# Performance work log

Measured on AMD Instinct MI355X. Metric: run time of the kernel, lower is better.

## Reference

```python
import jax, jax.numpy as jnp
import numpy as np

E, H, B, S = 512, 8, 8, 1024  # embed_dim, n_head, batch, n_agent (sequence)
DH = E // H
DECAY_SCALING = 1.0


def _rmsnorm(x, scale, eps=1e-6):
    return x * jax.lax.rsqrt(jnp.mean(x * x, axis=-1, keepdims=True) + eps) * scale


def _groupnorm(y, scale, bias, n_head, eps=1e-5):
    # GroupNorm with num_groups = n_head over the feature axis (flax semantics).
    b, s, e = y.shape
    yg = y.reshape(b, s, n_head, e // n_head)
    mu = jnp.mean(yg, axis=-1, keepdims=True)
    var = jnp.var(yg, axis=-1, keepdims=True)
    yn = (yg - mu) * jax.lax.rsqrt(var + eps)
    return yn.reshape(b, s, e) * scale + bias


def _decay_kappas(n_head, scaling):
    # RetNet multi-scale decays: 1 - exp(linspace(log(1/32), log(1/512), H))
    k = 1.0 - jnp.exp(jnp.linspace(jnp.log(1.0 / 32.0), jnp.log(1.0 / 512.0), n_head))
    return (k * scaling).astype(jnp.float32)


def _msr(key_x, query_x, value_x, wq, wk, wv, wg, wo, gs, gb, kappas):
    # Parallel multi-scale retention (masked / causal, full_self_retention=False).
    b, s, e = query_x.shape
    h = wq.shape[0]
    q = jnp.einsum('bse,hed->bhsd', query_x, wq)
    k = jnp.einsum('bse,hed->bhsd', key_x, wk)
    v = jnp.einsum('bse,hed->bhsd', value_x, wv)
    n = jnp.arange(s)
    diff = n[:, None] - n[None, :]
    causal = diff >= 0
    expnt = jnp.where(causal, diff, 0).astype(q.dtype)
    # D[h,n,m] = kappa_h^(n-m) for n>=m else 0
    D = jnp.where(causal[None], kappas[:, None, None] ** expnt[None], 0.0)
    scores = jnp.einsum('bhnd,bhmd->bhnm', q, k) * D[None]  # [B,H,S,S]
    ret = jnp.einsum('bhnm,bhmd->bhnd', scores, v)
    ret = ret.transpose(0, 2, 1, 3).reshape(b, s, e)
    ret = _groupnorm(ret, gs, gb, h)
    return (jax.nn.swish(query_x @ wg) * ret) @ wo


def _swiglu(x, w_gate, w_lin, w_out):
    return (jax.nn.swish(x @ w_gate) * (x @ w_lin)) @ w_out


def setup_inputs() -> dict:
    key = jax.random.key(0)
    ks = jax.random.split(key, 20)
    sc = 0.02
    d = {
        'x': jax.random.normal(ks[0], (B, S, E), jnp.float32),
        'obs_rep': jax.random.normal(ks[1], (B, S, E), jnp.float32),
        # retention 1 params
        'wq1': jax.random.normal(ks[2], (H, E, DH), jnp.float32) * sc,
        'wk1': jax.random.normal(ks[3], (H, E, DH), jnp.float32) * sc,
        'wv1': jax.random.normal(ks[4], (H, E, DH), jnp.float32) * sc,
        'wg1': jax.random.normal(ks[5], (E, E), jnp.float32) * sc,
        'wo1': jax.random.normal(ks[6], (E, E), jnp.float32) * sc,
        'gs1': jnp.ones((E,), jnp.float32),
        'gb1': jnp.zeros((E,), jnp.float32),
        # retention 2 params
        'wq2': jax.random.normal(ks[7], (H, E, DH), jnp.float32) * sc,
        'wk2': jax.random.normal(ks[8], (H, E, DH), jnp.float32) * sc,
        'wv2': jax.random.normal(ks[9], (H, E, DH), jnp.float32) * sc,
        'wg2': jax.random.normal(ks[10], (E, E), jnp.float32) * sc,
        'wo2': jax.random.normal(ks[11], (E, E), jnp.float32) * sc,
        'gs2': jnp.ones((E,), jnp.float32),
        'gb2': jnp.zeros((E,), jnp.float32),
        # RMSNorm scales
        'ln1_s': jnp.ones((E,), jnp.float32),
        'ln2_s': jnp.ones((E,), jnp.float32),
        'ln3_s': jnp.ones((E,), jnp.float32),
        # SwiGLU(hidden=E, input=E)
        'ffn_w_lin': jax.random.normal(ks[12], (E, E), jnp.float32) * sc,
        'ffn_w_gate': jax.random.normal(ks[13], (E, E), jnp.float32) * sc,
        'ffn_w_out': jax.random.normal(ks[14], (E, E), jnp.float32) * sc,
    }
    return d


def reference(x, obs_rep, wq1, wk1, wv1, wg1, wo1, gs1, gb1,
              wq2, wk2, wv2, wg2, wo2, gs2, gb2,
              ln1_s, ln2_s, ln3_s, ffn_w_lin, ffn_w_gate, ffn_w_out):
    kappas = _decay_kappas(H, DECAY_SCALING)
    # x = ln1(x + retn1(key=x, query=x, value=x))
    x1 = _rmsnorm(x + _msr(x, x, x, wq1, wk1, wv1, wg1, wo1, gs1, gb1, kappas), ln1_s)
    # x = ln2(obs_rep + retn2(key=x1, query=obs_rep, value=x1))
    x2 = _rmsnorm(obs_rep + _msr(x1, obs_rep, x1, wq2, wk2, wv2, wg2, wo2, gs2, gb2, kappas), ln2_s)
    # out = ln3(x2 + ffn(x2))
    return _rmsnorm(x2 + _swiglu(x2, ffn_w_gate, ffn_w_lin, ffn_w_out), ln3_s)
```

## Files before the change

### kernel.cpp

```cpp
#include <hip/hip_runtime.h>
#include <hip/hip_bf16.h>
#include <stdint.h>

typedef unsigned short u16;
typedef unsigned int   u32;
typedef __bf16 bf16x8 __attribute__((ext_vector_type(8)));
typedef u16    u16x8  __attribute__((ext_vector_type(8)));
typedef float  f32x4  __attribute__((ext_vector_type(4)));

#define E_   512
#define H_   8
#define DH_  64
#define B_   8
#define S_   1024
#define M_   (B_ * S_)
#define NTOT (M_ * E_)

__device__ __forceinline__ u16 f2bf(float f) {
    u32 x = __float_as_uint(f);
    x += 0x7fffu + ((x >> 16) & 1u);
    return (u16)(x >> 16);
}
__device__ __forceinline__ float bf2f(u16 b) { return __uint_as_float((u32)b << 16); }
__device__ __forceinline__ bf16x8 as_bf(u16x8 v) {
// ... 16 lines not shown
__global__ __launch_bounds__(256) void prep_weights(
    const float* __restrict__ wq1, const float* __restrict__ wk1, const float* __restrict__ wv1,
    const float* __restrict__ wg1, const float* __restrict__ wq2, const float* __restrict__ wk2,
    const float* __restrict__ wv2, const float* __restrict__ wg2, const float* __restrict__ wgat,
    const float* __restrict__ wlin, const float* __restrict__ wo1, const float* __restrict__ wo2,
    const float* __restrict__ wout,
    u16* __restrict__ WC1, u16* __restrict__ WC2, u16* __restrict__ WF,
    u16* __restrict__ WO1t, u16* __restrict__ WO2t, u16* __restrict__ WOUt) {
    __shared__ float tle[64][65];
    const int rt = blockIdx.y, c0 = blockIdx.x * 64, tid = threadIdx.x;
    u16* dst; const float* src; int lr0; bool qkv = false; int nb0 = 0, h = 0;
    if (rt < 64) {
        bool s1 = rt < 32;
        dst = s1 ? WC1 : WC2;
        int r = (rt & 31) * 64; lr0 = r;
        if (r < 1536) {
            qkv = true; h = (r >> 6) & 7;
            src = (r < 512) ? (s1 ? wq1 : wq2) : (r < 1024) ? (s1 ? wk1 : wk2) : (s1 ? wv1 : wv2);
        } else { src = s1 ? wg1 : wg2; nb0 = r - 1536; }
    } else if (rt < 80) {
        dst = WF; int r = (rt - 64) * 64; lr0 = r;
        src = (r < 512) ? wgat : wlin; nb0 = r & 511;
    } else if (rt < 88) { dst = WO1t; lr0 = (rt - 80) * 64; src = wo1; nb0 = lr0; }
    else if (rt < 96)   { dst = WO2t; lr0 = (rt - 88) * 64; src = wo2; nb0 = lr0; }
    else                { dst = WOUt; lr0 = (rt - 96) * 64; src = wout; nb0 = lr0; }

    #pragma unroll
    for (int i = 0; i < 16; ++i) {
        int idx = i * 256 + tid, a = idx >> 6, b = idx & 63;
        tle[a][b] = qkv ? src[(size_t)(h * 512 + c0 + a) * 64 + b]
                        : src[(size_t)(c0 + a) * 512 + nb0 + b];
    }
    __syncthreads();
    #pragma unroll
    for (int i = 0; i < 16; ++i) {
        int idx = i * 256 + tid;
        dst[(size_t)(lr0 + (idx >> 6)) * 512 + c0 + (idx & 63)] = f2bf(tle[idx & 63][idx >> 6]);
    }
}

__global__ __launch_bounds__(256) void cvt_both(const float* __restrict__ x,
                                                const float* __restrict__ obs,
                                                u16* __restrict__ XB, u16* __restrict__ OB) {
    int i = blockIdx.x * 256 + threadIdx.x;
    float4 v = ((const float4*)x)[i];
    ushort4 o;
    o.x = f2bf(v.x); o.y = f2bf(v.y); o.z = f2bf(v.z); o.w = f2bf(v.w);
    ((ushort4*)XB)[i] = o;
    v = ((const float4*)obs)[i];
    o.x = f2bf(v.x); o.y = f2bf(v.y); o.z = f2bf(v.z); o.w = f2bf(v.w);
    ((ushort4*)OB)[i] = o;
}

__global__ __launch_bounds__(256) void gemm_qkvg(const u16* __restrict__ A1,
                                                 const u16* __restrict__ A2,
                                                 const u16* __restrict__ W,
                                                 u16* __restrict__ QB, u16* __restrict__ KB,
                                                 u16* __restrict__ KT, u16* __restrict__ VT,
                                                 u16* __restrict__ GB) {
    __shared__ u16 sh[16384];
    u16* Als = sh;
    u16* Bls = sh + 8192;
    const int tid = threadIdx.x;
    const int l = tid & 63, w = tid >> 6;
    const int wm = w & 1, wn = w >> 1;
    int bx, by; xcd_map(blockIdx.x, 1024, 16, bx, by);
    const int bm = by * 128, bn = bx * 128;
    const int which = bx >> 2;
    const u16* A = (which == 1 || which == 2) ? A2 : A1;

    size_t srcA[4], srcB[4]; int ldst[4];
    #pragma unroll
    for (int c = 0; c < 4; ++c) {
        int row = c * 32 + w * 8 + (l >> 3);
        int chs = (l & 7) ^ (row & 7);
        srcA[c] = (size_t)(bm + row) * E_ + chs * 8;
        srcB[c] = (size_t)(bn + row) * E_ + chs * 8;
        ldst[c] = c * 2048 + w * 512;
    }
    int aoff[2][4], boff[2][4];
    #pragma unroll
    for (int kk = 0; kk < 2; ++kk)
        #pragma unroll
        for (int f = 0; f < 4; ++f) {
            int ra = wm * 64 + f * 16 + (l & 15);
            int rb = wn * 64 + f * 16 + (l & 15);
            int ch = kk * 4 + (l >> 4);
            aoff[kk][f] = ra * 128 + ((ch ^ (ra & 7)) << 4);
            boff[kk][f] = rb * 128 + ((ch ^ (rb & 7)) << 4);
        }

    f32x4 acc[4][4] = {};
    for (int t = 0; t < 8; ++t) {
        const int k1 = t * 64;
        #pragma unroll
        for (int c = 0; c < 4; ++c) {
            gll16(A + srcA[c] + k1, &Als[ldst[c]]);
            gll16(W + srcB[c] + k1, &Bls[ldst[c]]);
        }
        __syncthreads();
        #pragma unroll
        for (int kk = 0; kk < 2; ++kk) {
            bf16x8 af[4], bfr[4];
            #pragma unroll
            for (int f = 0; f < 4; ++f) {
                af[f]  = as_bf(*(const u16x8*)((const char*)Als + aoff[kk][f]));
                bfr[f] = as_bf(*(const u16x8*)((const char*)Bls + boff[kk][f]));
            }
            #pragma unroll
            for (int m = 0; m < 4; ++m)
                #pragma unroll
                for (int n = 0; n < 4; ++n)
                    acc[m][n] = __builtin_amdgcn_mfma_f32_16x16x32_bf16(af[m], bfr[n], acc[m][n], 0, 0, 0);
        }
        __syncthreads();
    }

    if (which != 2) {
        u16* dst = (which == 0) ? QB : (which == 1) ? KB : GB;
        #pragma unroll
        for (int m = 0; m < 4; ++m) {
            int row = bm + wm * 64 + m * 16 + ((l >> 4) << 2);
            #pragma unroll
            for (int n = 0; n < 4; ++n) {
                int coll = (bn & 511) + wn * 64 + n * 16 + (l & 15);
                f32x4 v = acc[m][n];
                #pragma unroll
                for (int r = 0; r < 4; ++r) dst[(size_t)(row + r) * E_ + coll] = f2bf(v[r]);
            }
        }
    }
    if (which == 1 || which == 2) {
        u16* dstT = (which == 2) ? VT : KT;
        #pragma unroll
        for (int m = 0; m < 4; ++m) {
            int row0 = wm * 64 + m * 16 + ((l >> 4) << 2);
            #pragma unroll
            for (int n = 0; n < 4; ++n) {
                int c = wn * 64 + n * 16 + (l & 15);
                f32x4 v = acc[m][n];
                uint2 pk; pk.x = cvtpk(v[0], v[1]); pk.y = cvtpk(v[2], v[3]);
                int off = c * 256 + (((row0 >> 3) ^ (c & 7)) << 4) + ((row0 & 7) << 1);
                *(uint2*)((char*)sh + off) = pk;
            }
        }
        __syncthreads();
        int c = tid >> 1, half = tid & 1;
        int collg = (bn & 511) + c;
        int bh = ((bm >> 10) << 3) + (collg >> 6);
        size_t gb = ((size_t)bh * 64 + (collg & 63)) * 1024 + (bm & 1023) + half * 64;
        #pragma unroll
        for (int j = 0; j < 8; ++j) {
            int chunk = half * 8 + j;
            uint4 vv = *(const uint4*)((const char*)sh + c * 256 + ((chunk ^ (c & 7)) << 4));
            *(uint4*)(dstT + gb + j * 8) = vv;
        }
    }
}

__global__ __launch_bounds__(256) void state_u(const u16* __restrict__ KT,
                                               const u16* __restrict__ VT,
                                               u16* __restrict__ U) {
    const int id = blockIdx.x;
    const int bh = id >> 3, c = id & 7;
    const int h = bh & 7;
    const int l = threadIdx.x & 63, w = threadIdx.x >> 6;
    const float kappa = 1.0f - __expf(-3.46573590f + (float)h * -0.39608410f);
    const float log2k = log2f(kappa);
    const float ik = 1.0f / kappa;

    bf16x8 af[4];
    {
        size_t vbase = ((size_t)bh * 64 + (w * 16 + (l & 15))) * 1024 + c * 128 + ((l >> 4) << 3);
        #pragma unroll
        for (int kk = 0; kk < 4; ++kk)
            af[kk] = as_bf(*(const u16x8*)(VT + vbase + kk * 32));
    }

    f32x4 acc[4] = {};
    #pragma unroll
    for (int fd = 0; fd < 4; ++fd) {
        size_t kbase = ((size_t)bh * 64 + (fd * 16 + (l & 15))) * 1024 + c * 128 + ((l >> 4) << 3);
        #pragma unroll
        for (int kk = 0; kk < 4; ++kk) {
            u16x8 kv = *(const u16x8*)(KT + kbase + kk * 32);
            int mb = kk * 32 + ((l >> 4) << 3);
            float wj = exp2f((float)(127 - mb) * log2k);
            u16x8 kw;
            #pragma unroll
            for (int j = 0; j < 8; ++j) { kw[j] = f2bf(bf2f(kv[j]) * wj); wj *= ik; }
            acc[fd] = __builtin_amdgcn_mfma_f32_16x16x32_bf16(af[kk], as_bf(kw), acc[fd], 0, 0, 0);
        }
    }

    #pragma unroll
    for (int fd = 0; fd < 4; ++fd) {
        int dv = w * 16 + ((l >> 4) << 2);
        int dk = fd * 16 + (l & 15);
        size_t ub = ((size_t)id * 64 + dv) * 64 + dk;
        #pragma unroll
        for (int r = 0; r < 4; ++r) U[ub + (size_t)r * 64] = f2bf(acc[fd][r]);
    }
}

__global__ __launch_bounds__(256) void retention_chunk(
        const u16* __restrict__ Q, const u16* __restrict__ K,
        const u16* __restrict__ VT, const u16* __restrict__ U,
        const u16* __restrict__ G,
        const float* __restrict__ gs, const float* __restrict__ gb,
        u16* __restrict__ T) {
    __shared__ u16 Ks[128 * 64], Vts[64 * 128], Ps[128 * 64], Ss[64 * 64];
    const int tid = threadIdx.x;
    const int l = tid & 63, w = tid >> 6;
    const int id = blockIdx.x;
    const int bh = id >> 3, c = id & 7;
    const int h = bh & 7;
    const int n0 = c * 128;
    const size_t base = (size_t)(bh >> 3) * (S_ * E_) + h * DH_;

    const float kappa = 1.0f - __expf(-3.46573590f + (float)h * -0.39608410f);
    const float log2k = log2f(kappa);
    const float ik = 1.0f / kappa;
    const float ikp2 = ik * ik, ikp3 = ikp2 * ik;

    float gsv[4], gbv[4];
    #pragma unroll
    for (int fd = 0; fd < 4; ++fd) {
        gsv[fd] = gs[h * 64 + fd * 16 + (l & 15)];
        gbv[fd] = gb[h * 64 + fd * 16 + (l & 15)];
    }

    #pragma unroll
    for (int cc = 0; cc < 4; ++cc) {
        int row = cc * 32 + w * 8 + (l >> 3);
        int chs = (l & 7) ^ (row & 7);
        gll16(K + base + (size_t)(n0 + row) * E_ + chs * 8, &Ks[cc * 2048 + w * 512]);
        int d = cc * 16 + w * 4 + (l >> 4);
        int vch = (l & 15) ^ (d & 15);
        gll16(VT + ((size_t)bh * 64 + d) * 1024 + n0 + vch * 8, &Vts[cc * 2048 + w * 512]);
    }

    bf16x8 qf[2][2];
    #pragma unroll
    for (int kk = 0; kk < 2; ++kk)
        #pragma unroll
        for (int fn = 0; fn < 2; ++fn) {
            int n = n0 + fn * 64 + w * 16 + (l & 15);
            qf[kk][fn] = as_bf(*(const u16x8*)(Q + base + (size_t)n * E_ + kk * 32 + ((l >> 4) << 3)));
        }

    if (c > 0) {
        float accs[16];
        #pragma unroll
        for (int j = 0; j < 16; ++j) accs[j] = 0.f;
        const float kC = exp2f(128.0f * log2k);
        float wc = 1.0f;
        size_t ub = (size_t)bh * (8 * 4096) + tid * 16;
        for (int cp = c - 1; cp >= 0; --cp) {
            const u16* up = U + ub + (size_t)cp * 4096;
            u16x8 a = *(const u16x8*)up;
            u16x8 b = *(const u16x8*)(up + 8);
            #pragma unroll
            for (int j = 0; j < 8; ++j) {
                accs[j]     += bf2f(a[j]) * wc;
                accs[8 + j] += bf2f(b[j]) * wc;
            }
            wc *= kC;
        }
        int dv = tid >> 2, ch0 = (tid & 3) << 1;
        #pragma unroll
        for (int hh = 0; hh < 2; ++hh) {
            uint4 pk;
            pk.x = cvtpk(accs[hh * 8 + 0], accs[hh * 8 + 1]);
            pk.y = cvtpk(accs[hh * 8 + 2], accs[hh * 8 + 3]);
            pk.z = cvtpk(accs[hh * 8 + 4], accs[hh * 8 + 5]);
            pk.w = cvtpk(accs[hh * 8 + 6], accs[hh * 8 + 7]);
            *(uint4*)((char*)Ss + dv * 128 + (((ch0 + hh) ^ (dv & 7)) << 4)) = pk;
        }
    }
    __syncthreads();

    f32x4 acc[2][4] = {};

    if (c > 0) {
        __builtin_amdgcn_s_setprio(1);
        #pragma unroll
        for (int kk = 0; kk < 2; ++kk) {
            bf16x8 sf[4];
            #pragma unroll
            for (int fd = 0; fd < 4; ++fd) {
                int dv = fd * 16 + (l & 15);
                int ch = kk * 4 + (l >> 4);
                sf[fd] = as_bf(*(const u16x8*)((const char*)Ss + dv * 128 + ((ch ^ (dv & 7)) << 4)));
            }
            #pragma unroll
            for (int fn = 0; fn < 2; ++fn)
                #pragma unroll
                for (int fd = 0; fd < 4; ++fd)
                    acc[fn][fd] = __builtin_amdgcn_mfma_f32_16x16x32_bf16(qf[kk][fn], sf[fd], acc[fn][fd], 0, 0, 0);
        }
        __builtin_amdgcn_s_setprio(0);
        #pragma unroll
        for (int fn = 0; fn < 2; ++fn) {
            int nl0 = fn * 64 + w * 16 + ((l >> 4) << 2);
            float fr0 = exp2f((float)(nl0 + 1) * log2k);
            float fr1 = fr0 * kappa, fr2 = fr1 * kappa, fr3 = fr2 * kappa;
            #pragma unroll
            for (int fd = 0; fd < 4; ++fd) {
                acc[fn][fd][0] *= fr0; acc[fn][fd][1] *= fr1;
                acc[fn][fd][2] *= fr2; acc[fn][fd][3] *= fr3;
            }
        }
    }

    #pragma unroll
    for (int mh = 0; mh < 2; ++mh) {
        const int m0l = mh * 64;
        bf16x8 kf[2][4];
        #pragma unroll
        for (int kk = 0; kk < 2; ++kk)
            #pragma unroll
            for (int f = 0; f < 4; ++f) {
                int row = m0l + f * 16 + (l & 15);
                int ch = kk * 4 + (l >> 4);
                kf[kk][f] = as_bf(*(const u16x8*)((const char*)Ks + row * 128 + ((ch ^ (row & 7)) << 4)));
            }
        #pragma unroll
        for (int fn = 0; fn < 2; ++fn) {
            if (mh == 1 && fn == 0) continue;
            f32x4 s[4] = {};
            __builtin_amdgcn_s_setprio(1);
            #pragma unroll
            for (int kk = 0; kk < 2; ++kk)
// ... 25 lines not shown
                pk.x = cvtpk(p0, p1);
                pk.y = cvtpk(p2, p3);
                *(uint2*)((char*)Ps + byteoff) = pk;
            }
        }
        #pragma unroll
        for (int km = 0; km < 2; ++km) {
            bf16x8 pf[2];
            #pragma unroll
            for (int fn = 0; fn < 2; ++fn) {
                if (mh == 1 && fn == 0) continue;
                int row = fn * 64 + w * 16 + (l & 15);
                int ch = km * 4 + (l >> 4);
                pf[fn] = as_bf(*(const u16x8*)((const char*)Ps + row * 128 + ((ch ^ (row & 7)) << 4)));
            }
            __builtin_amdgcn_s_setprio(1);
            #pragma unroll
            for (int fd = 0; fd < 4; ++fd) {
                int d = fd * 16 + (l & 15);
                int mch = mh * 8 + km * 4 + (l >> 4);
                bf16x8 vfr = as_bf(*(const u16x8*)((const char*)Vts + d * 256 + ((mch ^ (d & 15)) << 4)));
                #pragma unroll
                for (int fn = 0; fn < 2; ++fn) {
                    if (mh == 1 && fn == 0) continue;
                    acc[fn][fd] = __builtin_amdgcn_mfma_f32_16x16x32_bf16(pf[fn], vfr, acc[fn][fd], 0, 0, 0);
                }
            }
            __builtin_amdgcn_s_setprio(0);
        }
    }

    #pragma unroll
    for (int fn = 0; fn < 2; ++fn) {
        #pragma unroll
        for (int r = 0; r < 4; ++r) {
            float s1 = 0.f, s2 = 0.f;
            #pragma unroll
            for (int fd = 0; fd < 4; ++fd) { float v = acc[fn][fd][r]; s1 += v; s2 += v * v; }
            #pragma unroll
            for (int off = 1; off < 16; off <<= 1) {
                s1 += __shfl_xor(s1, off, 64);
                s2 += __shfl_xor(s2, off, 64);
            }
            float mean = s1 * (1.f / 64.f);
            float var  = s2 * (1.f / 64.f) - mean * mean;
            float rinv = rsqrtf(var + 1e-5f);
            int rowg = n0 + fn * 64 + w * 16 + ((l >> 4) << 2) + r;
            size_t rb = base + (size_t)rowg * E_;
            #pragma unroll
            for (int fd = 0; fd < 4; ++fd) {
                int d = fd * 16 + (l & 15);
                float ny = (acc[fn][fd][r] - mean) * rinv;
                float rn = ny * gsv[fd] + gbv[fd];
                float g = bf2f(G[rb + d]);
                T[rb + d] = f2bf(g * rn / (1.f + __expf(-g)));
            }
        }
    }
}

__global__ __launch_bounds__(256) void gemm_wo(const u16* __restrict__ A,
                                               const u16* __restrict__ W,
                                               u16* __restrict__ Cb) {
    __shared__ u16 Als[64 * 64];
    __shared__ u16 Bls[128 * 64];
    const int tid = threadIdx.x;
    const int l = tid & 63, w = tid >> 6;
    const int wm = w & 1, wn = w >> 1;
    int bx, by; xcd_map(blockIdx.x, 512, 4, bx, by);
    const int bm = by * 64, bn = bx * 128;

    size_t srcA[2], srcB[4]; int ldstA[2], ldstB[4];
    #pragma unroll
    for (int c = 0; c < 4; ++c) {
        int row = c * 32 + w * 8 + (l >> 3);
        int chs = (l & 7) ^ (row & 7);
        if (c < 2) { srcA[c] = (size_t)(bm + row) * E_ + chs * 8; ldstA[c] = c * 2048 + w * 512; }
        srcB[c] = (size_t)(bn + row) * E_ + chs * 8;
        ldstB[c] = c * 2048 + w * 512;
    }
    int aoff[2][2], boff[2][4];
    #pragma unroll
    for (int kk = 0; kk < 2; ++kk) {
        #pragma unroll
        for (int f = 0; f < 2; ++f) {
            int ra = wm * 32 + f * 16 + (l & 15);
            aoff[kk][f] = ra * 128 + (((kk * 4 + (l >> 4)) ^ (ra & 7)) << 4);
        }
        #pragma unroll
        for (int f = 0; f < 4; ++f) {
            int rb = wn * 64 + f * 16 + (l & 15);
            boff[kk][f] = rb * 128 + (((kk * 4 + (l >> 4)) ^ (rb & 7)) << 4);
        }
    }

    f32x4 acc[2][4] = {};
    for (int t = 0; t < 8; ++t) {
        const int k1 = t * 64;
        #pragma unroll
        for (int c = 0; c < 2; ++c) gll16(A + srcA[c] + k1, &Als[ldstA[c]]);
        #pragma unroll
        for (int c = 0; c < 4; ++c) gll16(W + srcB[c] + k1, &Bls[ldstB[c]]);
        __syncthreads();
        #pragma unroll
        for (int kk = 0; kk < 2; ++kk) {
            bf16x8 af[2], bfr[4];
            #pragma unroll
            for (int f = 0; f < 2; ++f) af[f] = as_bf(*(const u16x8*)((const char*)Als + aoff[kk][f]));
            #pragma unroll
            for (int f = 0; f < 4; ++f) bfr[f] = as_bf(*(const u16x8*)((const char*)Bls + boff[kk][f]));
            #pragma unroll
            for (int m = 0; m < 2; ++m)
                #pragma unroll
                for (int n = 0; n < 4; ++n)
                    acc[m][n] = __builtin_amdgcn_mfma_f32_16x16x32_bf16(af[m], bfr[n], acc[m][n], 0, 0, 0);
        }
        __syncthreads();
    }

    #pragma unroll
    for (int m = 0; m < 2; ++m) {
        int row = bm + wm * 32 + m * 16 + ((l >> 4) << 2);
        #pragma unroll
        for (int n = 0; n < 4; ++n) {
            int col = bn + wn * 64 + n * 16 + (l & 15);
            f32x4 v = acc[m][n];
            #pragma unroll
            for (int r = 0; r < 4; ++r) Cb[(size_t)(row + r) * E_ + col] = f2bf(v[r]);
        }
    }
}

__global__ __launch_bounds__(256) void gemm_ffn(const u16* __restrict__ A,
                                                const u16* __restrict__ W,
                                                u16* __restrict__ T) {
    __shared__ u16 Als[64 * 64];
    __shared__ u16 Bgs[64 * 64];
    __shared__ u16 Bls[64 * 64];
    const int tid = threadIdx.x;
    const int l = tid & 63, w = tid >> 6;
    const int wm = w & 1, wn = w >> 1;
    int bx, by; xcd_map(blockIdx.x, 1024, 8, bx, by);
    const int bm = by * 64, bn = bx * 64;

    size_t srcA[2], srcG[2], srcL[2]; int ldst[2];
    #pragma unroll
    for (int c = 0; c < 2; ++c) {
        int row = c * 32 + w * 8 + (l >> 3);
        int chs = (l & 7) ^ (row & 7);
        srcA[c] = (size_t)(bm + row) * E_ + chs * 8;
        srcG[c] = (size_t)(bn + row) * E_ + chs * 8;
        srcL[c] = (size_t)(512 + bn + row) * E_ + chs * 8;
        ldst[c] = c * 2048 + w * 512;
    }
    int aoff[2][2], goff[2][2];
    #pragma unroll
    for (int kk = 0; kk < 2; ++kk)
        #pragma unroll
        for (int f = 0; f < 2; ++f) {
            int ra = wm * 32 + f * 16 + (l & 15);
            int rb = wn * 32 + f * 16 + (l & 15);
            aoff[kk][f] = ra * 128 + (((kk * 4 + (l >> 4)) ^ (ra & 7)) << 4);
            goff[kk][f] = rb * 128 + (((kk * 4 + (l >> 4)) ^ (rb & 7)) << 4);
        }

    f32x4 accg[2][2] = {}, accl[2][2] = {};
    for (int t = 0; t < 8; ++t) {
        const int k1 = t * 64;
        #pragma unroll
        for (int c = 0; c < 2; ++c) {
            gll16(A + srcA[c] + k1, &Als[ldst[c]]);
            gll16(W + srcG[c] + k1, &Bgs[ldst[c]]);
            gll16(W + srcL[c] + k1, &Bls[ldst[c]]);
        }
        __syncthreads();
        #pragma unroll
        for (int kk = 0; kk < 2; ++kk) {
            bf16x8 af[2], bg[2], bl[2];
            #pragma unroll
            for (int f = 0; f < 2; ++f) {
                af[f] = as_bf(*(const u16x8*)((const char*)Als + aoff[kk][f]));
                bg[f] = as_bf(*(const u16x8*)((const char*)Bgs + goff[kk][f]));
                bl[f] = as_bf(*(const u16x8*)((const char*)Bls + goff[kk][f]));
            }
            #pragma unroll
            for (int m = 0; m < 2; ++m)
                #pragma unroll
                for (int n = 0; n < 2; ++n) {
                    accg[m][n] = __builtin_amdgcn_mfma_f32_16x16x32_bf16(af[m], bg[n], accg[m][n], 0, 0, 0);
                    accl[m][n] = __builtin_amdgcn_mfma_f32_16x16x32_bf16(af[m], bl[n], accl[m][n], 0, 0, 0);
                }
        }
        __syncthreads();
    }

    #pragma unroll
    for (int m = 0; m < 2; ++m) {
        int row = bm + wm * 32 + m * 16 + ((l >> 4) << 2);
        #pragma unroll
        for (int n = 0; n < 2; ++n) {
            int col = bn + wn * 32 + n * 16 + (l & 15);
            #pragma unroll
            for (int r = 0; r < 4; ++r) {
                float g = accg[m][n][r], lv = accl[m][n][r];
                T[(size_t)(row + r) * E_ + col] = f2bf(g * lv / (1.f + __expf(-g)));
            }
        }
    }
}

__global__ __launch_bounds__(512) void rmsnorm_res(const float* __restrict__ Xf,
                                                   const u16* __restrict__ Xb,
                                                   const u16* __restrict__ Yb,
                                                   const float* __restrict__ sc,
                                                   float* __restrict__ outf,
                                                   u16* __restrict__ outb) {
    __shared__ float part[8];
    size_t row = blockIdx.x;
    int t = threadIdx.x;
    float xv = Xf ? Xf[row * E_ + t] : bf2f(Xb[row * E_ + t]);
    float v = xv + bf2f(Yb[row * E_ + t]);
    float sq = v * v;
    #pragma unroll
    for (int off = 1; off < 64; off <<= 1) sq += __shfl_xor(sq, off, 64);
    if ((t & 63) == 0) part[t >> 6] = sq;
    __syncthreads();
    float tot = 0.0f;
    #pragma unroll
    for (int i = 0; i < 8; ++i) tot += part[i];
    float r = rsqrtf(tot * (1.0f / 512.0f) + 1e-6f);
    float o = v * r * sc[t];
    if (outf) outf[row * E_ + t] = o;
    if (outb) outb[row * E_ + t] = f2bf(o);
}

extern "C" void kernel_launch(void* const* d_in, const int* in_sizes, int n_in,
                              void* d_out, int out_size, void* d_ws, size_t ws_size,
                              hipStream_t stream) {
    const float* x    = (const float*)d_in[0];
    const float* obs  = (const float*)d_in[1];
    const float* wq1  = (const float*)d_in[2];
    const float* wk1  = (const float*)d_in[3];
    const float* wv1  = (const float*)d_in[4];
    const float* wg1  = (const float*)d_in[5];
    const float* wo1  = (const float*)d_in[6];
    const float* gs1  = (const float*)d_in[7];
    const float* gb1  = (const float*)d_in[8];
    const float* wq2  = (const float*)d_in[9];
    const float* wk2  = (const float*)d_in[10];
    const float* wv2  = (const float*)d_in[11];
    const float* wg2  = (const float*)d_in[12];
    const float* wo2  = (const float*)d_in[13];
    const float* gs2  = (const float*)d_in[14];
    const float* gb2  = (const float*)d_in[15];
    const float* ln1s = (const float*)d_in[16];
    const float* ln2s = (const float*)d_in[17];
    const float* ln3s = (const float*)d_in[18];
    const float* wlin = (const float*)d_in[19];
    const float* wgat = (const float*)d_in[20];
    const float* wout = (const float*)d_in[21];

    u16* wsb = (u16*)d_ws;
    u16* WC1  = wsb;
    u16* WC2  = WC1 + 2048 * 512;
    u16* WF   = WC2 + 2048 * 512;
    u16* WO1t = WF + 1024 * 512;
    u16* WO2t = WO1t + 512 * 512;
    u16* WOUt = WO2t + 512 * 512;
    u16* XB   = WOUt + 512 * 512;
    u16* OB   = XB + NTOT;
    u16* QB   = OB + NTOT;
    u16* KB   = QB + NTOT;
    u16* KT   = KB + NTOT;
    u16* VT   = KT + NTOT;
    u16* GB   = VT + NTOT;
    u16* TB   = GB + NTOT;
    u16* UB   = TB + NTOT;
    u16* YB   = QB;

    dim3 tG(256);

    prep_weights<<<dim3(8, 104), tG, 0, stream>>>(wq1, wk1, wv1, wg1, wq2, wk2, wv2, wg2,
                                                  wgat, wlin, wo1, wo2, wout,
                                                  WC1, WC2, WF, WO1t, WO2t, WOUt);
    cvt_both<<<NTOT / 1024, tG, 0, stream>>>(x, obs, XB, OB);

    gemm_qkvg<<<1024, tG, 0, stream>>>(XB, XB, WC1, QB, KB, KT, VT, GB);
    state_u<<<512, tG, 0, stream>>>(KT, VT, UB);
    retention_chunk<<<512, tG, 0, stream>>>(QB, KB, VT, UB, GB, gs1, gb1, TB);
    gemm_wo<<<512, tG, 0, stream>>>(TB, WO1t, YB);
    rmsnorm_res<<<M_, 512, 0, stream>>>(x, nullptr, YB, ln1s, nullptr, XB);

    gemm_qkvg<<<1024, tG, 0, stream>>>(OB, XB, WC2, QB, KB, KT, VT, GB);
    state_u<<<512, tG, 0, stream>>>(KT, VT, UB);
    retention_chunk<<<512, tG, 0, stream>>>(QB, KB, VT, UB, GB, gs2, gb2, TB);
    gemm_wo<<<512, tG, 0, stream>>>(TB, WO2t, YB);
    rmsnorm_res<<<M_, 512, 0, stream>>>(obs, nullptr, YB, ln2s, nullptr, OB);

    gemm_ffn<<<1024, tG, 0, stream>>>(OB, WF, TB);
    gemm_wo<<<512, tG, 0, stream>>>(TB, WOUt, YB);
    rmsnorm_res<<<M_, 512, 0, stream>>>(nullptr, OB, YB, ln3s, (float*)d_out, nullptr);
}
```

Baseline: 204.4 us.

## Fuse output projection GEMM with residual add and RMSNorm epilogue

Replaces the separate output-projection GEMM and row-wise RMSNorm kernels with one kernel. Each block computes full 512-wide rows for 32 rows, adds the residual and reduces the sum of squares across warps in shared memory, then writes the normalized output directly. This removes the intermediate bf16 projection buffer round trip and three kernel launches. In exchange it uses a large 64KB weight tile in LDS, launches only 256 blocks with lower occupancy, and adds MFMA priority hints.

```diff
diff --git a/kernel.cpp b/kernel.cpp
--- a/kernel.cpp
+++ b/kernel.cpp
@@ -457,74 +457,112 @@
     }
 }
 
-__global__ __launch_bounds__(256) void gemm_wo(const u16* __restrict__ A,
-                                               const u16* __restrict__ W,
-                                               u16* __restrict__ Cb) {
-    __shared__ u16 Als[64 * 64];
-    __shared__ u16 Bls[128 * 64];
+__global__ __launch_bounds__(256) void gemm_wo_rms(const u16* __restrict__ A,
+                                                   const u16* __restrict__ W,
+                                                   const float* __restrict__ Xf,
+                                                   const u16* __restrict__ Xb,
+                                                   const float* __restrict__ sc,
+                                                   float* __restrict__ outf,
+                                                   u16* __restrict__ outb) {
+    __shared__ u16 Bls[512 * 64];
+    __shared__ u16 Als[32 * 64];
+    __shared__ float red[4][32];
     const int tid = threadIdx.x;
     const int l = tid & 63, w = tid >> 6;
-    const int wm = w & 1, wn = w >> 1;
-    int bx, by; xcd_map(blockIdx.x, 512, 4, bx, by);
-    const int bm = by * 64, bn = bx * 128;
-
-    size_t srcA[2], srcB[4]; int ldstA[2], ldstB[4];
-    #pragma unroll
-    for (int c = 0; c < 4; ++c) {
+    const int bm = blockIdx.x * 32;
+
+    int arow = w * 8 + (l >> 3);
+    size_t srcA = (size_t)(bm + arow) * E_ + (((l & 7) ^ (arow & 7)) * 8);
+    int ldstA = w * 512;
+    size_t srcB[16]; int ldstB[16];
+    #pragma unroll
+    for (int c = 0; c < 16; ++c) {
         int row = c * 32 + w * 8 + (l >> 3);
-        int chs = (l & 7) ^ (row & 7);
-        if (c < 2) { srcA[c] = (size_t)(bm + row) * E_ + chs * 8; ldstA[c] = c * 2048 + w * 512; }
-        srcB[c] = (size_t)(bn + row) * E_ + chs * 8;
+        srcB[c] = (size_t)row * E_ + (((l & 7) ^ (row & 7)) * 8);
         ldstB[c] = c * 2048 + w * 512;
     }
-    int aoff[2][2], boff[2][4];
+    int aoff[2][2], boff[2][8];
     #pragma unroll
     for (int kk = 0; kk < 2; ++kk) {
         #pragma unroll
-        for (int f = 0; f < 2; ++f) {
-            int ra = wm * 32 + f * 16 + (l & 15);
-            aoff[kk][f] = ra * 128 + (((kk * 4 + (l >> 4)) ^ (ra & 7)) << 4);
-        }
-        #pragma unroll
-        for (int f = 0; f < 4; ++f) {
-            int rb = wn * 64 + f * 16 + (l & 15);
-            boff[kk][f] = rb * 128 + (((kk * 4 + (l >> 4)) ^ (rb & 7)) << 4);
-        }
-    }
-
-    f32x4 acc[2][4] = {};
+        for (int mi = 0; mi < 2; ++mi) {
+            int ra = mi * 16 + (l & 15);
+            aoff[kk][mi] = ra * 128 + (((kk * 4 + (l >> 4)) ^ (ra & 7)) << 4);
+        }
+        #pragma unroll
+        for (int n = 0; n < 8; ++n) {
+            int rb = w * 128 + n * 16 + (l & 15);
+            boff[kk][n] = rb * 128 + (((kk * 4 + (l >> 4)) ^ (rb & 7)) << 4);
+        }
+    }
+
+    f32x4 acc[2][8] = {};
     for (int t = 0; t < 8; ++t) {
         const int k1 = t * 64;
-        #pragma unroll
-        for (int c = 0; c < 2; ++c) gll16(A + srcA[c] + k1, &Als[ldstA[c]]);
-        #pragma unroll
-        for (int c = 0; c < 4; ++c) gll16(W + srcB[c] + k1, &Bls[ldstB[c]]);
+        gll16(A + srcA + k1, &Als[ldstA]);
+        #pragma unroll
+        for (int c = 0; c < 16; ++c) gll16(W + srcB[c] + k1, &Bls[ldstB[c]]);
         __syncthreads();
         #pragma unroll
         for (int kk = 0; kk < 2; ++kk) {
-            bf16x8 af[2], bfr[4];
-            #pragma unroll
-            for (int f = 0; f < 2; ++f) af[f] = as_bf(*(const u16x8*)((const char*)Als + aoff[kk][f]));
-            #pragma unroll
-            for (int f = 0; f < 4; ++f) bfr[f] = as_bf(*(const u16x8*)((const char*)Bls + boff[kk][f]));
-            #pragma unroll
-            for (int m = 0; m < 2; ++m)
+            bf16x8 af[2], bfr[8];
+            #pragma unroll
+            for (int mi = 0; mi < 2; ++mi)
+                af[mi] = as_bf(*(const u16x8*)((const char*)Als + aoff[kk][mi]));
+            #pragma unroll
+            for (int n = 0; n < 8; ++n)
+                bfr[n] = as_bf(*(const u16x8*)((const char*)Bls + boff[kk][n]));
+            __builtin_amdgcn_s_setprio(1);
+            #pragma unroll
+            for (int mi = 0; mi < 2; ++mi)
                 #pragma unroll
-                for (int n = 0; n < 4; ++n)
-                    acc[m][n] = __builtin_amdgcn_mfma_f32_16x16x32_bf16(af[m], bfr[n], acc[m][n], 0, 0, 0);
+                for (int n = 0; n < 8; ++n)
+                    acc[mi][n] = __builtin_amdgcn_mfma_f32_16x16x32_bf16(af[mi], bfr[n], acc[mi][n], 0, 0, 0);
+            __builtin_amdgcn_s_setprio(0);
         }
         __syncthreads();
     }
 
-    #pragma unroll
-    for (int m = 0; m < 2; ++m) {
-        int row = bm + wm * 32 + m * 16 + ((l >> 4) << 2);
-        #pragma unroll
-        for (int n = 0; n < 4; ++n) {
-            int col = bn + wn * 64 + n * 16 + (l & 15);
-            f32x4 v = acc[m][n];
-            #pragma unroll
-            for (int r = 0; r < 4; ++r) Cb[(size_t)(row + r) * E_ + col] = f2bf(v[r]);
+    float scv[8];
+    #pragma unroll
+    for (int n = 0; n < 8; ++n) scv[n] = sc[w * 128 + n * 16 + (l & 15)];
+
+    #pragma unroll
+    for (int mi = 0; mi < 2; ++mi) {
+        #pragma unroll
+        for (int r = 0; r < 4; ++r) {
+            int rowl = mi * 16 + ((l >> 4) << 2) + r;
+            size_t rb = (size_t)(bm + rowl) * E_;
+            float part = 0.f;
+            #pragma unroll
+            for (int n = 0; n < 8; ++n) {
+                int col = w * 128 + n * 16 + (l & 15);
+                float xv = Xf ? Xf[rb + col] : bf2f(Xb[rb + col]);
+                float v = acc[mi][n][r] + xv;
+                acc[mi][n][r] = v;
+                part += v * v;
+            }
+            #pragma unroll
+            for (int off = 1; off < 16; off <<= 1) part += __shfl_xor(part, off, 64);
+            if ((l & 15) == 0) red[w][rowl] = part;
+        }
+    }
+    __syncthreads();
+    #pragma unroll
+    for (int mi = 0; mi < 2; ++mi) {
+        #pragma unroll
+        for (int r = 0; r < 4; ++r) {
+            int rowl = mi * 16 + ((l >> 4) << 2) + r;
+            float sigma = red[0][rowl] + red[1][rowl] + red[2][rowl] + red[3][rowl];
+            float rinv = rsqrtf(sigma * (1.0f / 512.0f) + 1e-6f);
+            size_t rb = (size_t)(bm + rowl) * E_;
+            #pragma unroll
+            for (int n = 0; n < 8; ++n) {
+                int col = w * 128 + n * 16 + (l & 15);
+                float o = acc[mi][n][r] * rinv * scv[n];
+                if (outf) outf[rb + col] = o;
+                if (outb) outb[rb + col] = f2bf(o);
+            }
         }
     }
 }
@@ -605,31 +643,6 @@
             }
         }
     }
-}
-
-__global__ __launch_bounds__(512) void rmsnorm_res(const float* __restrict__ Xf,
-                                                   const u16* __restrict__ Xb,
-                                                   const u16* __restrict__ Yb,
-                                                   const float* __restrict__ sc,
-                                                   float* __restrict__ outf,
-                                                   u16* __restrict__ outb) {
-    __shared__ float part[8];
-    size_t row = blockIdx.x;
-    int t = threadIdx.x;
-    float xv = Xf ? Xf[row * E_ + t] : bf2f(Xb[row * E_ + t]);
-    float v = xv + bf2f(Yb[row * E_ + t]);
-    float sq = v * v;
-    #pragma unroll
-    for (int off = 1; off < 64; off <<= 1) sq += __shfl_xor(sq, off, 64);
-    if ((t & 63) == 0) part[t >> 6] = sq;
-    __syncthreads();
-    float tot = 0.0f;
-    #pragma unroll
-    for (int i = 0; i < 8; ++i) tot += part[i];
-    float r = rsqrtf(tot * (1.0f / 512.0f) + 1e-6f);
-    float o = v * r * sc[t];
-    if (outf) outf[row * E_ + t] = o;
-    if (outb) outb[row * E_ + t] = f2bf(o);
 }
 
 extern "C" void kernel_launch(void* const* d_in, const int* in_sizes, int n_in,
@@ -674,7 +687,6 @@
     u16* GB   = VT + NTOT;
     u16* TB   = GB + NTOT;
     u16* UB   = TB + NTOT;
-    u16* YB   = QB;
 
     dim3 tG(256);
 
@@ -686,16 +698,13 @@
     gemm_qkvg<<<1024, tG, 0, stream>>>(XB, XB, WC1, QB, KB, KT, VT, GB);
     state_u<<<512, tG, 0, stream>>>(KT, VT, UB);
     retention_chunk<<<512, tG, 0, stream>>>(QB, KB, VT, UB, GB, gs1, gb1, TB);
-    gemm_wo<<<512, tG, 0, stream>>>(TB, WO1t, YB);
-    rmsnorm_res<<<M_, 512, 0, stream>>>(x, nullptr, YB, ln1s, nullptr, XB);
+    gemm_wo_rms<<<256, tG, 0, stream>>>(TB, WO1t, x, nullptr, ln1s, nullptr, XB);
 
     gemm_qkvg<<<1024, tG, 0, stream>>>(OB, XB, WC2, QB, KB, KT, VT, GB);
     state_u<<<512, tG, 0, stream>>>(KT, VT, UB);
     retention_chunk<<<512, tG, 0, stream>>>(QB, KB, VT, UB, GB, gs2, gb2, TB);
-    gemm_wo<<<512, tG, 0, stream>>>(TB, WO2t, YB);
-    rmsnorm_res<<<M_, 512, 0, stream>>>(obs, nullptr, YB, ln2s, nullptr, OB);
+    gemm_wo_rms<<<256, tG, 0, stream>>>(TB, WO2t, obs, nullptr, ln2s, nullptr, OB);
 
     gemm_ffn<<<1024, tG, 0, stream>>>(OB, WF, TB);
-    gemm_wo<<<512, tG, 0, stream>>>(TB, WOUt, YB);
-    rmsnorm_res<<<M_, 512, 0, stream>>>(nullptr, OB, YB, ln3s, (float*)d_out, nullptr);
-}
+    gemm_wo_rms<<<256, tG, 0, stream>>>(TB, WOUt, nullptr, OB, ln3s, (float*)d_out, nullptr);
+}
```

Result: no change. 207.6 us (+1.6%).

## Fuse Q and gate projections into retention kernel; vectorize RMSNorm

Applied to the files above, without the earlier changes.

Removes Q and gate outputs from the projection GEMM, which now computes only K and V. Each retention block computes its own Q and gate tiles with MFMA directly from the bf16 activations and weights, keeping the gate in registers. This removes two intermediate tensor round-trips through global memory, at the cost of unstaged global loads inside the retention kernel. RMSNorm is rewritten to process one row per wavefront with 8-wide vector loads, and it reads the bf16 residual copy instead of the fp32 input, trading a little precision for less traffic.

```diff
diff --git a/kernel.cpp b/kernel.cpp
--- a/kernel.cpp
+++ b/kernel.cpp
@@ -92,22 +92,22 @@
     ((ushort4*)OB)[i] = o;
 }
 
-__global__ __launch_bounds__(256) void gemm_qkvg(const u16* __restrict__ A1,
-                                                 const u16* __restrict__ A2,
-                                                 const u16* __restrict__ W,
-                                                 u16* __restrict__ QB, u16* __restrict__ KB,
-                                                 u16* __restrict__ KT, u16* __restrict__ VT,
-                                                 u16* __restrict__ GB) {
+__global__ __launch_bounds__(256) void gemm_kv(const u16* __restrict__ A,
+                                               const u16* __restrict__ W,
+                                               u16* __restrict__ KB,
+                                               u16* __restrict__ KT,
+                                               u16* __restrict__ VT) {
     __shared__ u16 sh[16384];
     u16* Als = sh;
     u16* Bls = sh + 8192;
     const int tid = threadIdx.x;
     const int l = tid & 63, w = tid >> 6;
     const int wm = w & 1, wn = w >> 1;
-    int bx, by; xcd_map(blockIdx.x, 1024, 16, bx, by);
-    const int bm = by * 128, bn = bx * 128;
+    int bx, by; xcd_map(blockIdx.x, 512, 8, bx, by);
+    const int bm = by * 128;
+    const int bnl = (bx & 3) * 128;
     const int which = bx >> 2;
-    const u16* A = (which == 1 || which == 2) ? A2 : A1;
+    const int wrow0 = 512 + which * 512 + bnl;
 
     size_t srcA[4], srcB[4]; int ldst[4];
     #pragma unroll
@@ -115,7 +115,7 @@
         int row = c * 32 + w * 8 + (l >> 3);
         int chs = (l & 7) ^ (row & 7);
         srcA[c] = (size_t)(bm + row) * E_ + chs * 8;
-        srcB[c] = (size_t)(bn + row) * E_ + chs * 8;
+        srcB[c] = (size_t)(wrow0 + row) * E_ + chs * 8;
         ldst[c] = c * 2048 + w * 512;
     }
     int aoff[2][4], boff[2][4];
@@ -156,22 +156,21 @@
         __syncthreads();
     }
 
-    if (which != 2) {
-        u16* dst = (which == 0) ? QB : (which == 1) ? KB : GB;
+    if (which == 0) {
         #pragma unroll
         for (int m = 0; m < 4; ++m) {
             int row = bm + wm * 64 + m * 16 + ((l >> 4) << 2);
             #pragma unroll
             for (int n = 0; n < 4; ++n) {
-                int coll = (bn & 511) + wn * 64 + n * 16 + (l & 15);
+                int coll = bnl + wn * 64 + n * 16 + (l & 15);
                 f32x4 v = acc[m][n];
                 #pragma unroll
-                for (int r = 0; r < 4; ++r) dst[(size_t)(row + r) * E_ + coll] = f2bf(v[r]);
-            }
-        }
-    }
-    if (which == 1 || which == 2) {
-        u16* dstT = (which == 2) ? VT : KT;
+                for (int r = 0; r < 4; ++r) KB[(size_t)(row + r) * E_ + coll] = f2bf(v[r]);
+            }
+        }
+    }
+    {
+        u16* dstT = which ? VT : KT;
         #pragma unroll
         for (int m = 0; m < 4; ++m) {
             int row0 = wm * 64 + m * 16 + ((l >> 4) << 2);
@@ -186,7 +185,7 @@
         }
         __syncthreads();
         int c = tid >> 1, half = tid & 1;
-        int collg = (bn & 511) + c;
+        int collg = bnl + c;
         int bh = ((bm >> 10) << 3) + (collg >> 6);
         size_t gb = ((size_t)bh * 64 + (collg & 63)) * 1024 + (bm & 1023) + half * 64;
         #pragma unroll
@@ -244,19 +243,20 @@
 }
 
 __global__ __launch_bounds__(256) void retention_chunk(
-        const u16* __restrict__ Q, const u16* __restrict__ K,
-        const u16* __restrict__ VT, const u16* __restrict__ U,
-        const u16* __restrict__ G,
+        const u16* __restrict__ XQ, const u16* __restrict__ WQG,
+        const u16* __restrict__ K, const u16* __restrict__ VT,
+        const u16* __restrict__ U,
         const float* __restrict__ gs, const float* __restrict__ gb,
         u16* __restrict__ T) {
-    __shared__ u16 Ks[128 * 64], Vts[64 * 128], Ps[128 * 64], Ss[64 * 64];
+    __shared__ u16 Ks[128 * 64], Vts[64 * 128], Ps[128 * 64], Ss[64 * 64], Qs[128 * 64];
     const int tid = threadIdx.x;
     const int l = tid & 63, w = tid >> 6;
     const int id = blockIdx.x;
     const int bh = id >> 3, c = id & 7;
     const int h = bh & 7;
     const int n0 = c * 128;
-    const size_t base = (size_t)(bh >> 3) * (S_ * E_) + h * DH_;
+    const size_t base  = (size_t)(bh >> 3) * (S_ * E_) + h * DH_;
+    const size_t xbase = (size_t)(bh >> 3) * (S_ * E_);
 
     const float kappa = 1.0f - __expf(-3.46573590f + (float)h * -0.39608410f);
     const float log2k = log2f(kappa);
@@ -280,13 +280,43 @@
         gll16(VT + ((size_t)bh * 64 + d) * 1024 + n0 + vch * 8, &Vts[cc * 2048 + w * 512]);
     }
 
-    bf16x8 qf[2][2];
-    #pragma unroll
-    for (int kk = 0; kk < 2; ++kk)
-        #pragma unroll
-        for (int fn = 0; fn < 2; ++fn) {
-            int n = n0 + fn * 64 + w * 16 + (l & 15);
-            qf[kk][fn] = as_bf(*(const u16x8*)(Q + base + (size_t)n * E_ + kk * 32 + ((l >> 4) << 3)));
+    f32x4 qacc[2][4] = {}, gacc[2][4] = {};
+    {
+        const u16* xr0 = XQ + xbase + (size_t)(n0 + w * 16 + (l & 15)) * E_ + ((l >> 4) << 3);
+        const u16* xr1 = xr0 + (size_t)64 * E_;
+        const u16* wq0 = WQG + (size_t)(h * 64 + (l & 15)) * E_ + ((l >> 4) << 3);
+        const u16* wg0 = wq0 + (size_t)1536 * E_;
+        for (int kk = 0; kk < 16; ++kk) {
+            const int kof = kk * 32;
+            bf16x8 ax0 = as_bf(*(const u16x8*)(xr0 + kof));
+            bf16x8 ax1 = as_bf(*(const u16x8*)(xr1 + kof));
+            __builtin_amdgcn_s_setprio(1);
+            #pragma unroll
+            for (int fd = 0; fd < 4; ++fd) {
+                bf16x8 bq = as_bf(*(const u16x8*)(wq0 + (size_t)(fd * 16) * E_ + kof));
+                qacc[0][fd] = __builtin_amdgcn_mfma_f32_16x16x32_bf16(ax0, bq, qacc[0][fd], 0, 0, 0);
+                qacc[1][fd] = __builtin_amdgcn_mfma_f32_16x16x32_bf16(ax1, bq, qacc[1][fd], 0, 0, 0);
+            }
+            #pragma unroll
+            for (int fd = 0; fd < 4; ++fd) {
+                bf16x8 bg = as_bf(*(const u16x8*)(wg0 + (size_t)(fd * 16) * E_ + kof));
+                gacc[0][fd] = __builtin_amdgcn_mfma_f32_16x16x32_bf16(ax0, bg, gacc[0][fd], 0, 0, 0);
+                gacc[1][fd] = __builtin_amdgcn_mfma_f32_16x16x32_bf16(ax1, bg, gacc[1][fd], 0, 0, 0);
+            }
+            __builtin_amdgcn_s_setprio(0);
+        }
+    }
+    #pragma unroll
+    for (int fn = 0; fn < 2; ++fn)
+        #pragma unroll
+        for (int fd = 0; fd < 4; ++fd) {
+            #pragma unroll
+            for (int r = 0; r < 4; ++r) {
+                int n = fn * 64 + w * 16 + ((l >> 4) << 2) + r;
+                int dk = fd * 16 + (l & 15);
+                int off = n * 128 + (((dk >> 3) ^ (n & 7)) << 4) + ((dk & 7) << 1);
+                *(u16*)((char*)Qs + off) = f2bf(qacc[fn][fd][r]);
+            }
         }
 
     if (c > 0) {
@@ -319,6 +349,16 @@
         }
     }
     __syncthreads();
+
+    bf16x8 qf[2][2];
+    #pragma unroll
+    for (int kk = 0; kk < 2; ++kk)
+        #pragma unroll
+        for (int fn = 0; fn < 2; ++fn) {
+            int n = fn * 64 + w * 16 + (l & 15);
+            int ck = kk * 4 + (l >> 4);
+            qf[kk][fn] = as_bf(*(const u16x8*)((const char*)Qs + n * 128 + ((ck ^ (n & 7)) << 4)));
+        }
 
     f32x4 acc[2][4] = {};
 
@@ -450,7 +490,7 @@
                 int d = fd * 16 + (l & 15);
                 float ny = (acc[fn][fd][r] - mean) * rinv;
                 float rn = ny * gsv[fd] + gbv[fd];
-                float g = bf2f(G[rb + d]);
+                float g = gacc[fn][fd][r];
                 T[rb + d] = f2bf(g * rn / (1.f + __expf(-g)));
             }
         }
@@ -607,29 +647,38 @@
     }
 }
 
-__global__ __launch_bounds__(512) void rmsnorm_res(const float* __restrict__ Xf,
-                                                   const u16* __restrict__ Xb,
+__global__ __launch_bounds__(256) void rmsnorm_res(const u16* __restrict__ Xb,
                                                    const u16* __restrict__ Yb,
                                                    const float* __restrict__ sc,
                                                    float* __restrict__ outf,
                                                    u16* __restrict__ outb) {
-    __shared__ float part[8];
-    size_t row = blockIdx.x;
-    int t = threadIdx.x;
-    float xv = Xf ? Xf[row * E_ + t] : bf2f(Xb[row * E_ + t]);
-    float v = xv + bf2f(Yb[row * E_ + t]);
-    float sq = v * v;
-    #pragma unroll
-    for (int off = 1; off < 64; off <<= 1) sq += __shfl_xor(sq, off, 64);
-    if ((t & 63) == 0) part[t >> 6] = sq;
-    __syncthreads();
-    float tot = 0.0f;
-    #pragma unroll
-    for (int i = 0; i < 8; ++i) tot += part[i];
-    float r = rsqrtf(tot * (1.0f / 512.0f) + 1e-6f);
-    float o = v * r * sc[t];
-    if (outf) outf[row * E_ + t] = o;
-    if (outb) outb[row * E_ + t] = f2bf(o);
+    int row = blockIdx.x * 4 + (threadIdx.x >> 6);
+    int l = threadIdx.x & 63;
+    size_t off = (size_t)row * E_ + l * 8;
+    u16x8 xv = *(const u16x8*)(Xb + off);
+    u16x8 yv = *(const u16x8*)(Yb + off);
+    float v[8]; float sq = 0.f;
+    #pragma unroll
+    for (int j = 0; j < 8; ++j) { v[j] = bf2f(xv[j]) + bf2f(yv[j]); sq += v[j] * v[j]; }
+    #pragma unroll
+    for (int o = 1; o < 64; o <<= 1) sq += __shfl_xor(sq, o, 64);
+    float rinv = rsqrtf(sq * (1.0f / 512.0f) + 1e-6f);
+    float4 s0 = ((const float4*)sc)[l * 2];
+    float4 s1 = ((const float4*)sc)[l * 2 + 1];
+    float sv[8] = {s0.x, s0.y, s0.z, s0.w, s1.x, s1.y, s1.z, s1.w};
+    if (outb) {
+        u16x8 o8;
+        #pragma unroll
+        for (int j = 0; j < 8; ++j) o8[j] = f2bf(v[j] * rinv * sv[j]);
+        *(u16x8*)(outb + off) = o8;
+    }
+    if (outf) {
+        float4 o0, o1;
+        o0.x = v[0]*rinv*sv[0]; o0.y = v[1]*rinv*sv[1]; o0.z = v[2]*rinv*sv[2]; o0.w = v[3]*rinv*sv[3];
+        o1.x = v[4]*rinv*sv[4]; o1.y = v[5]*rinv*sv[5]; o1.z = v[6]*rinv*sv[6]; o1.w = v[7]*rinv*sv[7];
+        ((float4*)(outf))[(off >> 2)]     = o0;
+        ((float4*)(outf))[(off >> 2) + 1] = o1;
+    }
 }
 
 extern "C" void kernel_launch(void* const* d_in, const int* in_sizes, int n_in,
@@ -667,14 +716,12 @@
     u16* WOUt = WO2t + 512 * 512;
     u16* XB   = WOUt + 512 * 512;
     u16* OB   = XB + NTOT;
-    u16* QB   = OB + NTOT;
-    u16* KB   = QB + NTOT;
+    u16* KB   = OB + NTOT;
     u16* KT   = KB + NTOT;
     u16* VT   = KT + NTOT;
-    u16* GB   = VT + NTOT;
-    u16* TB   = GB + NTOT;
+    u16* TB   = VT + NTOT;
     u16* UB   = TB + NTOT;
-    u16* YB   = QB;
+    u16* YB   = UB + 64 * 8 * 64 * 64;
 
     dim3 tG(256);
 
@@ -683,19 +730,19 @@
                                                   WC1, WC2, WF, WO1t, WO2t, WOUt);
     cvt_both<<<NTOT / 1024, tG, 0, stream>>>(x, obs, XB, OB);
 
-    gemm_qkvg<<<1024, tG, 0, stream>>>(XB, XB, WC1, QB, KB, KT, VT, GB);
+    gemm_kv<<<512, tG, 0, stream>>>(XB, WC1, KB, KT, VT);
     state_u<<<512, tG, 0, stream>>>(KT, VT, UB);
-    retention_chunk<<<512, tG, 0, stream>>>(QB, KB, VT, UB, GB, gs1, gb1, TB);
+    retention_chunk<<<512, tG, 0, stream>>>(XB, WC1, KB, VT, UB, gs1, gb1, TB);
     gemm_wo<<<512, tG, 0, stream>>>(TB, WO1t, YB);
-    rmsnorm_res<<<M_, 512, 0, stream>>>(x, nullptr, YB, ln1s, nullptr, XB);
-
-    gemm_qkvg<<<1024, tG, 0, stream>>>(OB, XB, WC2, QB, KB, KT, VT, GB);
+    rmsnorm_res<<<M_ / 4, tG, 0, stream>>>(XB, YB, ln1s, nullptr, XB);
+
+    gemm_kv<<<512, tG, 0, stream>>>(XB, WC2, KB, KT, VT);
     state_u<<<512, tG, 0, stream>>>(KT, VT, UB);
-    retention_chunk<<<512, tG, 0, stream>>>(QB, KB, VT, UB, GB, gs2, gb2, TB);
+    retention_chunk<<<512, tG, 0, stream>>>(OB, WC2, KB, VT, UB, gs2, gb2, TB);
     gemm_wo<<<512, tG, 0, stream>>>(TB, WO2t, YB);
-    rmsnorm_res<<<M_, 512, 0, stream>>>(obs, nullptr, YB, ln2s, nullptr, OB);
+    rmsnorm_res<<<M_ / 4, tG, 0, stream>>>(OB, YB, ln2s, nullptr, OB);
 
     gemm_ffn<<<1024, tG, 0, stream>>>(OB, WF, TB);
     gemm_wo<<<512, tG, 0, stream>>>(TB, WOUt, YB);
-    rmsnorm_res<<<M_, 512, 0, stream>>>(nullptr, OB, YB, ln3s, (float*)d_out, nullptr);
-}
+    rmsnorm_res<<<M_ / 4, tG, 0, stream>>>(OB, YB, ln3s, (float*)d_out, nullptr);
+}
```

New measurement: 224.4 us. +9.8%, slower.

## Double-buffer LDS in QKVG GEMM and vectorize RMSNorm to wave-per-row

Applied to the files above, without the earlier changes.

The QKVG GEMM now uses two LDS buffers. The next K-tile is prefetched with async global-to-LDS loads while MFMAs run on the current tile, with explicit vmcnt waits and setprio around the MFMAs. The RMSNorm kernel is rewritten so each 64-lane wave handles one row with 8-wide vector loads and no shared-memory reduction. The residual now comes from the bf16 copies instead of the fp32 inputs, which slightly reduces precision. LDS usage per GEMM block doubles, which may lower occupancy.

```diff
diff --git a/kernel.cpp b/kernel.cpp
--- a/kernel.cpp
+++ b/kernel.cpp
@@ -98,9 +98,7 @@
                                                  u16* __restrict__ QB, u16* __restrict__ KB,
                                                  u16* __restrict__ KT, u16* __restrict__ VT,
                                                  u16* __restrict__ GB) {
-    __shared__ u16 sh[16384];
-    u16* Als = sh;
-    u16* Bls = sh + 8192;
+    __shared__ u16 sh[32768];
     const int tid = threadIdx.x;
     const int l = tid & 63, w = tid >> 6;
     const int wm = w & 1, wn = w >> 1;
@@ -131,29 +129,51 @@
         }
 
     f32x4 acc[4][4] = {};
+    #pragma unroll
+    for (int c = 0; c < 4; ++c) {
+        gll16(A + srcA[c], &sh[ldst[c]]);
+        gll16(W + srcB[c], &sh[16384 + ldst[c]]);
+    }
+
     for (int t = 0; t < 8; ++t) {
-        const int k1 = t * 64;
-        #pragma unroll
-        for (int c = 0; c < 4; ++c) {
-            gll16(A + srcA[c] + k1, &Als[ldst[c]]);
-            gll16(W + srcB[c] + k1, &Bls[ldst[c]]);
-        }
-        __syncthreads();
+        const int cur = t & 1;
+        if (t < 7) {
+            const int k1 = (t + 1) * 64;
+            const int nb = (cur ^ 1) * 8192;
+            #pragma unroll
+            for (int c = 0; c < 4; ++c) {
+                gll16(A + srcA[c] + k1, &sh[nb + ldst[c]]);
+                gll16(W + srcB[c] + k1, &sh[16384 + nb + ldst[c]]);
+            }
+            asm volatile("s_waitcnt vmcnt(8)" ::: "memory");
+        } else {
+            asm volatile("s_waitcnt vmcnt(0)" ::: "memory");
+        }
+        __builtin_amdgcn_sched_barrier(0);
+        __builtin_amdgcn_s_barrier();
+
+        const char* ab = (const char*)sh + cur * 16384;
+        const char* bb = (const char*)sh + 32768 + cur * 16384;
         #pragma unroll
         for (int kk = 0; kk < 2; ++kk) {
             bf16x8 af[4], bfr[4];
             #pragma unroll
             for (int f = 0; f < 4; ++f) {
-                af[f]  = as_bf(*(const u16x8*)((const char*)Als + aoff[kk][f]));
-                bfr[f] = as_bf(*(const u16x8*)((const char*)Bls + boff[kk][f]));
-            }
+                af[f]  = as_bf(*(const u16x8*)(ab + aoff[kk][f]));
+                bfr[f] = as_bf(*(const u16x8*)(bb + boff[kk][f]));
+            }
+            __builtin_amdgcn_s_setprio(1);
             #pragma unroll
             for (int m = 0; m < 4; ++m)
                 #pragma unroll
                 for (int n = 0; n < 4; ++n)
                     acc[m][n] = __builtin_amdgcn_mfma_f32_16x16x32_bf16(af[m], bfr[n], acc[m][n], 0, 0, 0);
-        }
-        __syncthreads();
+            __builtin_amdgcn_s_setprio(0);
+        }
+        if (t < 7) {
+            __builtin_amdgcn_s_barrier();
+            __builtin_amdgcn_sched_barrier(0);
+        }
     }
 
     if (which != 2) {
@@ -172,6 +192,7 @@
     }
     if (which == 1 || which == 2) {
         u16* dstT = (which == 2) ? VT : KT;
+        __syncthreads();
         #pragma unroll
         for (int m = 0; m < 4; ++m) {
             int row0 = wm * 64 + m * 16 + ((l >> 4) << 2);
@@ -607,29 +628,38 @@
     }
 }
 
-__global__ __launch_bounds__(512) void rmsnorm_res(const float* __restrict__ Xf,
-                                                   const u16* __restrict__ Xb,
+__global__ __launch_bounds__(256) void rmsnorm_res(const u16* __restrict__ Xb,
                                                    const u16* __restrict__ Yb,
                                                    const float* __restrict__ sc,
                                                    float* __restrict__ outf,
                                                    u16* __restrict__ outb) {
-    __shared__ float part[8];
-    size_t row = blockIdx.x;
-    int t = threadIdx.x;
-    float xv = Xf ? Xf[row * E_ + t] : bf2f(Xb[row * E_ + t]);
-    float v = xv + bf2f(Yb[row * E_ + t]);
-    float sq = v * v;
-    #pragma unroll
-    for (int off = 1; off < 64; off <<= 1) sq += __shfl_xor(sq, off, 64);
-    if ((t & 63) == 0) part[t >> 6] = sq;
-    __syncthreads();
-    float tot = 0.0f;
-    #pragma unroll
-    for (int i = 0; i < 8; ++i) tot += part[i];
-    float r = rsqrtf(tot * (1.0f / 512.0f) + 1e-6f);
-    float o = v * r * sc[t];
-    if (outf) outf[row * E_ + t] = o;
-    if (outb) outb[row * E_ + t] = f2bf(o);
+    int row = blockIdx.x * 4 + (threadIdx.x >> 6);
+    int l = threadIdx.x & 63;
+    size_t off = (size_t)row * E_ + l * 8;
+    u16x8 xv = *(const u16x8*)(Xb + off);
+    u16x8 yv = *(const u16x8*)(Yb + off);
+    float v[8]; float sq = 0.f;
+    #pragma unroll
+    for (int j = 0; j < 8; ++j) { v[j] = bf2f(xv[j]) + bf2f(yv[j]); sq += v[j] * v[j]; }
+    #pragma unroll
+    for (int o = 1; o < 64; o <<= 1) sq += __shfl_xor(sq, o, 64);
+    float rinv = rsqrtf(sq * (1.0f / 512.0f) + 1e-6f);
+    float4 s0 = ((const float4*)sc)[l * 2];
+    float4 s1 = ((const float4*)sc)[l * 2 + 1];
+    float sv[8] = {s0.x, s0.y, s0.z, s0.w, s1.x, s1.y, s1.z, s1.w};
+    if (outb) {
+        u16x8 o8;
+        #pragma unroll
+        for (int j = 0; j < 8; ++j) o8[j] = f2bf(v[j] * rinv * sv[j]);
+        *(u16x8*)(outb + off) = o8;
+    }
+    if (outf) {
+        float4 o0, o1;
+        o0.x = v[0]*rinv*sv[0]; o0.y = v[1]*rinv*sv[1]; o0.z = v[2]*rinv*sv[2]; o0.w = v[3]*rinv*sv[3];
+        o1.x = v[4]*rinv*sv[4]; o1.y = v[5]*rinv*sv[5]; o1.z = v[6]*rinv*sv[6]; o1.w = v[7]*rinv*sv[7];
+        ((float4*)(outf))[(off >> 2)]     = o0;
+        ((float4*)(outf))[(off >> 2) + 1] = o1;
+    }
 }
 
 extern "C" void kernel_launch(void* const* d_in, const int* in_sizes, int n_in,
@@ -687,15 +717,15 @@
     state_u<<<512, tG, 0, stream>>>(KT, VT, UB);
     retention_chunk<<<512, tG, 0, stream>>>(QB, KB, VT, UB, GB, gs1, gb1, TB);
     gemm_wo<<<512, tG, 0, stream>>>(TB, WO1t, YB);
-    rmsnorm_res<<<M_, 512, 0, stream>>>(x, nullptr, YB, ln1s, nullptr, XB);
+    rmsnorm_res<<<M_ / 4, tG, 0, stream>>>(XB, YB, ln1s, nullptr, XB);
 
     gemm_qkvg<<<1024, tG, 0, stream>>>(OB, XB, WC2, QB, KB, KT, VT, GB);
     state_u<<<512, tG, 0, stream>>>(KT, VT, UB);
     retention_chunk<<<512, tG, 0, stream>>>(QB, KB, VT, UB, GB, gs2, gb2, TB);
     gemm_wo<<<512, tG, 0, stream>>>(TB, WO2t, YB);
-    rmsnorm_res<<<M_, 512, 0, stream>>>(obs, nullptr, YB, ln2s, nullptr, OB);
+    rmsnorm_res<<<M_ / 4, tG, 0, stream>>>(OB, YB, ln2s, nullptr, OB);
 
     gemm_ffn<<<1024, tG, 0, stream>>>(OB, WF, TB);
     gemm_wo<<<512, tG, 0, stream>>>(TB, WOUt, YB);
-    rmsnorm_res<<<M_, 512, 0, stream>>>(nullptr, OB, YB, ln3s, (float*)d_out, nullptr);
-}
+    rmsnorm_res<<<M_ / 4, tG, 0, stream>>>(OB, YB, ln3s, (float*)d_out, nullptr);
+}
```

Measured after the change: 172.9 us. 1.18x faster.
